# Optimization experiments

Hardware: AMD Instinct MI355X
Metric: run time of the kernel (lower is better)

Reference implementation:

```python
import jax, jax.numpy as jnp
import numpy as np

KSIZE = 3
RES_SCALE = 0.2
WITH_RESIDUAL = True


def setup_inputs() -> dict:
    key = jax.random.key(0)
    x = jax.random.normal(key, (8, 3, 1024, 1024), dtype=jnp.float32)
    return {"x": x}


def reference(x) -> jnp.ndarray:
    B, C, H, W = x.shape
    k = KSIZE
    p = k // 2
    # zero padding matches F.unfold(padding=k//2)
    xp = jnp.pad(x, ((0, 0), (0, 0), (p, p), (p, p)))
    # [B, C, k*k, H, W] stack of shifted views (k*k = 9, small static loop)
    patches = jnp.stack(
        [xp[:, :, di:di + H, dj:dj + W] for di in range(k) for dj in range(k)],
        axis=2,
    )
    # median of odd-sized window = middle element of sorted values
    med = jnp.sort(patches, axis=2)[:, :, (k * k) // 2]
    if WITH_RESIDUAL:
        return x + RES_SCALE * (med - x)
    return med
```

## Files before the change

kernel.cpp:

```cpp
#include <hip/hip_runtime.h>


#define S2(a, b) { float _t = fminf(a, b); b = fmaxf(a, b); a = _t; }

__device__ __forceinline__ float med3f(float a, float b, float c) {
    return fmaxf(fminf(a, b), fminf(fmaxf(a, b), c));
}

__global__ __launch_bounds__(256) void median_blur_kernel(
    const float* __restrict__ xin, float* __restrict__ out, int H, int W)
{
    const int tx = threadIdx.x;
    const int x0 = tx << 2;
    const int y  = blockIdx.x;
    const int z  = blockIdx.y;
    const size_t plane = (size_t)z * H * W;
    const float* base = xin + plane;

    float t[6], m[6], b[6];

    {
        const float* row = base + (size_t)y * W;
        const float4 c = *reinterpret_cast<const float4*>(row + x0);
        m[0] = (x0 > 0)     ? row[x0 - 1] : 0.0f;
        m[1] = c.x; m[2] = c.y; m[3] = c.z; m[4] = c.w;
        m[5] = (x0 + 4 < W) ? row[x0 + 4] : 0.0f;
    }
    if (y > 0) {
        const float* row = base + (size_t)(y - 1) * W;
        const float4 c = *reinterpret_cast<const float4*>(row + x0);
        t[0] = (x0 > 0)     ? row[x0 - 1] : 0.0f;
        t[1] = c.x; t[2] = c.y; t[3] = c.z; t[4] = c.w;
        t[5] = (x0 + 4 < W) ? row[x0 + 4] : 0.0f;
    } else {
        t[0] = t[1] = t[2] = t[3] = t[4] = t[5] = 0.0f;
    }
    if (y + 1 < H) {
        const float* row = base + (size_t)(y + 1) * W;
        const float4 c = *reinterpret_cast<const float4*>(row + x0);
        b[0] = (x0 > 0)     ? row[x0 - 1] : 0.0f;
        b[1] = c.x; b[2] = c.y; b[3] = c.z; b[4] = c.w;
        b[5] = (x0 + 4 < W) ? row[x0 + 4] : 0.0f;
    } else {
        b[0] = b[1] = b[2] = b[3] = b[4] = b[5] = 0.0f;
    }

    const float origs[4] = { m[1], m[2], m[3], m[4] };

    float lo[6], mi[6], hi[6];
#pragma unroll
    for (int j = 0; j < 6; ++j) {
        float a = t[j], c0 = m[j], d = b[j];
        S2(a, c0); S2(c0, d); S2(a, c0);
        lo[j] = a; mi[j] = c0; hi[j] = d;
    }

    float4 o;
    float* op = &o.x;
#pragma unroll
    for (int j = 0; j < 4; ++j) {
        float mxlo = fmaxf(lo[j], fmaxf(lo[j + 1], lo[j + 2]));
        float mnhi = fminf(hi[j], fminf(hi[j + 1], hi[j + 2]));
        float mdmi = med3f(mi[j], mi[j + 1], mi[j + 2]);
        float med  = med3f(mxlo, mdmi, mnhi);
        float xc   = origs[j];
        op[j] = xc + 0.2f * (med - xc);
    }
    *reinterpret_cast<float4*>(out + plane + (size_t)y * W + x0) = o;
}

extern "C" void kernel_launch(void* const* d_in, const int* in_sizes, int n_in,
                              void* d_out, int out_size, void* d_ws, size_t ws_size,
                              hipStream_t stream) {
    const float* x = (const float*)d_in[0];
    float* out = (float*)d_out;
    const int H = 1024, W = 1024;
    const int planes = in_sizes[0] / (H * W);
    dim3 block(256);
    dim3 grid(H, planes);
    median_blur_kernel<<<grid, block, 0, stream>>>(x, out, H, W);
}
```

Before: 184.6 us.

## Process 16 rows per block with sliding row window and wave shuffles for halos

Each block now walks 16 consecutive rows and keeps a rolling three-row register window, so each input row is loaded once per block instead of three times. Horizontal halo values are taken from neighbouring lanes with shuffles instead of separate scalar loads, and only wave-edge lanes still read from memory. This reduces redundant global and L2 traffic and per-block launch overhead. The cost is fewer blocks (64x24) and a serial per-thread dependency chain across rows, which may expose more load latency.

Measured after the change: 182.1 us. No clear change (-1.3%).

```diff
diff --git a/kernel.cpp b/kernel.cpp
--- a/kernel.cpp
+++ b/kernel.cpp
@@ -7,66 +7,73 @@
     return fmaxf(fminf(a, b), fminf(fmaxf(a, b), c));
 }
 
+constexpr int ROWS = 16;
+
 __global__ __launch_bounds__(256) void median_blur_kernel(
-    const float* __restrict__ xin, float* __restrict__ out, int H, int W)
+    const float* __restrict__ xin, float* __restrict__ out)
 {
-    const int tx = threadIdx.x;
-    const int x0 = tx << 2;
-    const int y  = blockIdx.x;
-    const int z  = blockIdx.y;
+    const int W = 1024, H = 1024;
+    const int tx   = threadIdx.x;
+    const int lane = tx & 63;
+    const int x0   = tx << 2;
+    const int y0   = blockIdx.x * ROWS;
+    const int z    = blockIdx.y;
     const size_t plane = (size_t)z * H * W;
-    const float* base = xin + plane;
+    const float* base  = xin + plane;
+    float*       obase = out + plane;
 
     float t[6], m[6], b[6];
 
-    {
+    auto load_row = [&](int y, float* dst) {
+        if (y < 0 || y >= H) {
+#pragma unroll
+            for (int j = 0; j < 6; ++j) dst[j] = 0.0f;
+            return;
+        }
         const float* row = base + (size_t)y * W;
-        const float4 c = *reinterpret_cast<const float4*>(row + x0);
-        m[0] = (x0 > 0)     ? row[x0 - 1] : 0.0f;
-        m[1] = c.x; m[2] = c.y; m[3] = c.z; m[4] = c.w;
-        m[5] = (x0 + 4 < W) ? row[x0 + 4] : 0.0f;
+        float4 c = *reinterpret_cast<const float4*>(row + x0);
+        float left  = __shfl_up(c.w, 1);
+        float right = __shfl_down(c.x, 1);
+        if (lane == 0)  left  = (x0 > 0)     ? row[x0 - 1] : 0.0f;
+        if (lane == 63) right = (x0 + 4 < W) ? row[x0 + 4] : 0.0f;
+        dst[0] = left; dst[1] = c.x; dst[2] = c.y; dst[3] = c.z; dst[4] = c.w; dst[5] = right;
+    };
+
+    load_row(y0 - 1, t);
+    load_row(y0,     m);
+    load_row(y0 + 1, b);
+
+#pragma unroll 4
+    for (int r = 0; r < ROWS; ++r) {
+        float nxt[6];
+        {
+            const int yn = (r < ROWS - 1) ? (y0 + r + 2) : H;
+            load_row(yn, nxt);
+        }
+
+        float lo[6], mi[6], hi[6];
+#pragma unroll
+        for (int j = 0; j < 6; ++j) {
+            float a = t[j], c0 = m[j], d = b[j];
+            S2(a, c0); S2(c0, d); S2(a, c0);
+            lo[j] = a; mi[j] = c0; hi[j] = d;
+        }
+
+        float4 o; float* op = &o.x;
+#pragma unroll
+        for (int j = 0; j < 4; ++j) {
+            float mxlo = fmaxf(lo[j], fmaxf(lo[j + 1], lo[j + 2]));
+            float mnhi = fminf(hi[j], fminf(hi[j + 1], hi[j + 2]));
+            float mdmi = med3f(mi[j], mi[j + 1], mi[j + 2]);
+            float med  = med3f(mxlo, mdmi, mnhi);
+            float xc   = m[j + 1];
+            op[j] = xc + 0.2f * (med - xc);
+        }
+        *reinterpret_cast<float4*>(obase + (size_t)(y0 + r) * W + x0) = o;
+
+#pragma unroll
+        for (int j = 0; j < 6; ++j) { t[j] = m[j]; m[j] = b[j]; b[j] = nxt[j]; }
     }
-    if (y > 0) {
-        const float* row = base + (size_t)(y - 1) * W;
-        const float4 c = *reinterpret_cast<const float4*>(row + x0);
-        t[0] = (x0 > 0)     ? row[x0 - 1] : 0.0f;
-        t[1] = c.x; t[2] = c.y; t[3] = c.z; t[4] = c.w;
-        t[5] = (x0 + 4 < W) ? row[x0 + 4] : 0.0f;
-    } else {
-        t[0] = t[1] = t[2] = t[3] = t[4] = t[5] = 0.0f;
-    }
-    if (y + 1 < H) {
-        const float* row = base + (size_t)(y + 1) * W;
-        const float4 c = *reinterpret_cast<const float4*>(row + x0);
-        b[0] = (x0 > 0)     ? row[x0 - 1] : 0.0f;
-        b[1] = c.x; b[2] = c.y; b[3] = c.z; b[4] = c.w;
-        b[5] = (x0 + 4 < W) ? row[x0 + 4] : 0.0f;
-    } else {
-        b[0] = b[1] = b[2] = b[3] = b[4] = b[5] = 0.0f;
-    }
-
-    const float origs[4] = { m[1], m[2], m[3], m[4] };
-
-    float lo[6], mi[6], hi[6];
-#pragma unroll
-    for (int j = 0; j < 6; ++j) {
-        float a = t[j], c0 = m[j], d = b[j];
-        S2(a, c0); S2(c0, d); S2(a, c0);
-        lo[j] = a; mi[j] = c0; hi[j] = d;
-    }
-
-    float4 o;
-    float* op = &o.x;
-#pragma unroll
-    for (int j = 0; j < 4; ++j) {
-        float mxlo = fmaxf(lo[j], fmaxf(lo[j + 1], lo[j + 2]));
-        float mnhi = fminf(hi[j], fminf(hi[j + 1], hi[j + 2]));
-        float mdmi = med3f(mi[j], mi[j + 1], mi[j + 2]);
-        float med  = med3f(mxlo, mdmi, mnhi);
-        float xc   = origs[j];
-        op[j] = xc + 0.2f * (med - xc);
-    }
-    *reinterpret_cast<float4*>(out + plane + (size_t)y * W + x0) = o;
 }
 
 extern "C" void kernel_launch(void* const* d_in, const int* in_sizes, int n_in,
@@ -77,6 +84,6 @@
     const int H = 1024, W = 1024;
     const int planes = in_sizes[0] / (H * W);
     dim3 block(256);
-    dim3 grid(H, planes);
-    median_blur_kernel<<<grid, block, 0, stream>>>(x, out, H, W);
+    dim3 grid(H / ROWS, planes);
+    median_blur_kernel<<<grid, block, 0, stream>>>(x, out);
 }
```
